# Optimization experiments

Measured on AMD Instinct MI355X. Metric: run time of the kernel, lower is better.

Reference implementation:

```python
import jax, jax.numpy as jnp
import numpy as np

HIDDEN = 2048
NUM_EXPERTS = 64
TOP_K = 8
EPS = 1e-6


def setup_inputs() -> dict:
    key = jax.random.key(0)
    k1, k2, k3, k4 = jax.random.split(key, 4)
    hidden_states = jax.random.normal(k1, (4, 4096, HIDDEN), dtype=jnp.float32)
    scale = jnp.ones((HIDDEN,), dtype=jnp.float32) + 0.01 * jax.random.normal(k2, (HIDDEN,), dtype=jnp.float32)
    proj_w = jax.random.normal(k3, (NUM_EXPERTS, HIDDEN), dtype=jnp.float32) * (HIDDEN ** -0.5)
    per_expert_scale = jnp.ones((NUM_EXPERTS,), dtype=jnp.float32) + 0.01 * jax.random.normal(k4, (NUM_EXPERTS,), dtype=jnp.float32)
    return {"hidden_states": hidden_states, "scale": scale, "proj_w": proj_w, "per_expert_scale": per_expert_scale}


def reference(hidden_states, scale, proj_w, per_expert_scale):
    H = hidden_states.shape[-1]
    # RMSNorm without learned scale
    x = hidden_states * jax.lax.rsqrt(jnp.mean(hidden_states * hidden_states, axis=-1, keepdims=True) + EPS)
    # elementwise scale and 1/sqrt(H) root-size scaling
    x = x * scale * (H ** -0.5)
    # router logits: [B,S,E]
    logits = jnp.einsum("bsh,eh->bse", x, proj_w)
    router_probs = jax.nn.softmax(logits.astype(jnp.float32), axis=-1)
    top_k_weights, top_k_index = jax.lax.top_k(router_probs, TOP_K)
    top_k_weights = top_k_weights / jnp.sum(top_k_weights, axis=-1, keepdims=True)
    top_k_weights = top_k_weights * per_expert_scale[top_k_index]
    # histc with bins=E, min=0, max=E on integer indices == bincount
    num_tokens_per_expert = jnp.bincount(top_k_index.reshape(-1), length=NUM_EXPERTS).astype(jnp.float32)
    return (top_k_weights.astype(hidden_states.dtype), top_k_index, num_tokens_per_expert)
```

## Files before the change

### kernel.cpp

```cpp
#include <hip/hip_runtime.h>
#include <math.h>

#define HIDDEN   2048
#define NEXPERT  64
#define TOPK     8
#define NTOK     16384
#define TOKB     16
#define CHUNK    256
#define NCHUNK   8
#define ROWP     264
#define RSQRT_H  0.02209708691207961
#define WSCALE   64.0f

typedef __attribute__((ext_vector_type(8))) _Float16 v8h;
typedef __attribute__((ext_vector_type(4))) float    v4f;

static __device__ __forceinline__ unsigned short f16b(float x) {
    return __builtin_bit_cast(unsigned short, (_Float16)x);
}
static __device__ __forceinline__ float f16f(unsigned short u) {
    return (float)__builtin_bit_cast(_Float16, u);
}

__global__ __launch_bounds__(256) void prep_wf(
    const float* __restrict__ w, const float* __restrict__ scale,
    unsigned short* __restrict__ wf)
{
    int i    = blockIdx.x * 256 + threadIdx.x;
    int j    = i & 7;
    int lane = (i >> 3) & 63;
    int nt   = (i >> 9) & 3;
    int ks   = i >> 11;
    int e    = nt * 16 + (lane & 15);
    int k    = ks * 32 + (lane >> 4) * 8 + j;
    float v  = w[e * HIDDEN + k] * scale[k] * WSCALE;
    unsigned short vh = f16b(v);
    unsigned short vl = f16b(v - f16f(vh));
    size_t base = (((size_t)(ks * 4 + nt) * 2) * 64 + lane) * 8 + j;
    wf[base]       = vh;
    wf[base + 512] = vl;
}

__global__ __launch_bounds__(256, 4) void router_main(
    const float* __restrict__ h, const unsigned short* __restrict__ wf,
    const float* __restrict__ pes,
    float* __restrict__ out_w, float* __restrict__ out_i, float* __restrict__ out_c)
{
    __shared__ __align__(16) char smem[34112];
    unsigned short* Xb0 = (unsigned short*)smem;
    float* lss = (float*)(smem + 33792);
    int*   hist = (int*)(smem + 33856);
    float* lg  = (float*)smem;

    const int tid  = (int)threadIdx.x;
    const int w    = __builtin_amdgcn_readfirstlane(tid >> 6);
    const int lane = tid & 63;
    const int m    = lane & 15;
    const int quad = lane >> 4;
    const int t0   = (int)blockIdx.x * TOKB;

    if (tid < NEXPERT) hist[tid] = 0;

    const int aoff = m * ROWP + quad * 8;

    v4f acc[4];
#pragma unroll
    for (int nt = 0; nt < 4; ++nt) acc[nt] = (v4f)0.f;
    float ss[4] = {0.f, 0.f, 0.f, 0.f};
    float4 st[4];

#pragma unroll
    for (int i = 0; i < 4; ++i) {
        int idx = i * 256 + tid, t = idx >> 6, kq = idx & 63;
        st[i] = *(const float4*)(h + (size_t)(t0 + t) * HIDDEN + kq * 4);
    }
#pragma unroll
    for (int i = 0; i < 4; ++i) {
        int idx = i * 256 + tid, t = idx >> 6, kq = idx & 63;
        float4 v = st[i];
        ss[i] = fmaf(v.x, v.x, fmaf(v.y, v.y, fmaf(v.z, v.z, fmaf(v.w, v.w, ss[i]))));
        unsigned short h0 = f16b(v.x), h1 = f16b(v.y), h2 = f16b(v.z), h3 = f16b(v.w);
        unsigned short l0 = f16b(v.x - f16f(h0)), l1 = f16b(v.y - f16f(h1));
        unsigned short l2 = f16b(v.z - f16f(h2)), l3 = f16b(v.w - f16f(h3));
        uint2 hp = make_uint2((unsigned)h0 | ((unsigned)h1 << 16),
                              (unsigned)h2 | ((unsigned)h3 << 16));
        uint2 lp = make_uint2((unsigned)l0 | ((unsigned)l1 << 16),
                              (unsigned)l2 | ((unsigned)l3 << 16));
        *(uint2*)(&Xb0[t * ROWP + kq * 4])        = hp;
        *(uint2*)(&Xb0[4224 + t * ROWP + kq * 4]) = lp;
    }

    for (int c = 0; c < NCHUNK; ++c) {
        __syncthreads();
        unsigned short* buf = Xb0 + (c & 1) * 8448;
        unsigned short* nbuf = Xb0 + ((c + 1) & 1) * 8448;

        if (c < NCHUNK - 1) {
#pragma unroll
            for (int i = 0; i < 4; ++i) {
                int idx = i * 256 + tid, t = idx >> 6, kq = idx & 63;
                st[i] = *(const float4*)(h + (size_t)(t0 + t) * HIDDEN
                                           + (c + 1) * CHUNK + kq * 4);
            }
        }

#pragma unroll
        for (int s = 0; s < 2; ++s) {
            const int ksl = 2 * w + s;
            const int ksg = c * 8 + ksl;
            v8h ah = *(const v8h*)(&buf[aoff + ksl * 32]);
            v8h al = *(const v8h*)(&buf[4224 + aoff + ksl * 32]);
#pragma unroll
            for (int nt = 0; nt < 4; ++nt) {
                const unsigned short* bp =
                    wf + (((size_t)(ksg * 4 + nt) * 2) * 64 + lane) * 8;
                v8h bh = *(const v8h*)bp;
                v8h bl = *(const v8h*)(bp + 512);
                acc[nt] = __builtin_amdgcn_mfma_f32_16x16x32_f16(ah, bh, acc[nt], 0, 0, 0);
                acc[nt] = __builtin_amdgcn_mfma_f32_16x16x32_f16(ah, bl, acc[nt], 0, 0, 0);
                acc[nt] = __builtin_amdgcn_mfma_f32_16x16x32_f16(al, bh, acc[nt], 0, 0, 0);
            }
        }

        if (c < NCHUNK - 1) {
#pragma unroll
            for (int i = 0; i < 4; ++i) {
                int idx = i * 256 + tid, t = idx >> 6, kq = idx & 63;
                float4 v = st[i];
                ss[i] = fmaf(v.x, v.x, fmaf(v.y, v.y, fmaf(v.z, v.z, fmaf(v.w, v.w, ss[i]))));
                unsigned short h0 = f16b(v.x), h1 = f16b(v.y), h2 = f16b(v.z), h3 = f16b(v.w);
                unsigned short l0 = f16b(v.x - f16f(h0)), l1 = f16b(v.y - f16f(h1));
                unsigned short l2 = f16b(v.z - f16f(h2)), l3 = f16b(v.w - f16f(h3));
                uint2 hp = make_uint2((unsigned)h0 | ((unsigned)h1 << 16),
                                      (unsigned)h2 | ((unsigned)h3 << 16));
                uint2 lp = make_uint2((unsigned)l0 | ((unsigned)l1 << 16),
                                      (unsigned)l2 | ((unsigned)l3 << 16));
                *(uint2*)(&nbuf[t * ROWP + kq * 4])        = hp;
                *(uint2*)(&nbuf[4224 + t * ROWP + kq * 4]) = lp;
            }
        }
    }

#pragma unroll
    for (int i = 0; i < 4; ++i) {
        float s = ss[i];
#pragma unroll
        for (int off = 32; off; off >>= 1) s += __shfl_xor(s, off, 64);
        if (lane == 0) lss[i * 4 + w] = s;
    }
    __syncthreads();

#pragma unroll
    for (int nt = 0; nt < 4; ++nt)
#pragma unroll
        for (int r = 0; r < 4; ++r) {
            int tl = quad * 4 + r;
            lg[(w * 16 + tl) * 65 + nt * 16 + m] = acc[nt][r];
        }
    __syncthreads();

    for (int i = 0; i < 4; ++i) {
        const int tok = w * 4 + i;
        float lsum = (lg[tok * 65 + lane]          + lg[1040 + tok * 65 + lane])
                   + (lg[2080 + tok * 65 + lane]   + lg[3120 + tok * 65 + lane]);
        double sst = (double)lss[tok];
        double rr  = 1.0 / sqrt(sst * (1.0 / (double)HIDDEN) + 1e-6);
        float logit = (float)((double)lsum * rr * (RSQRT_H / (double)WSCALE));

        float work = logit;
        float myval = 0.f; int myidx = 0; float m0 = 0.f;
#pragma unroll
        for (int j = 0; j < TOPK; ++j) {
            float mx = work;
#pragma unroll
            for (int off = 32; off; off >>= 1) mx = fmaxf(mx, __shfl_xor(mx, off, 64));
            unsigned long long msk = __ballot(work == mx);
            int src = __ffsll((long long)msk) - 1;
            if (j == 0) m0 = mx;
            if (lane == j) { myval = mx; myidx = src; }
            if (lane == src) work = -3.402823466e38f;
        }

        float ev = (lane < TOPK) ? expf(myval - m0) : 0.f;
        float es = ev;
        es += __shfl_xor(es, 1, 64);
        es += __shfl_xor(es, 2, 64);
        es += __shfl_xor(es, 4, 64);
        if (lane < TOPK) {
            float wgt = (ev / es) * pes[myidx];
            size_t o = (size_t)(t0 + tok) * TOPK + lane;
            out_w[o] = wgt;
            out_i[o] = (float)myidx;
            atomicAdd(&hist[myidx], 1);
        }
    }

    __syncthreads();
    if (tid < NEXPERT)
        atomicAdd(&out_c[tid], (float)hist[tid]);
}

extern "C" void kernel_launch(void* const* d_in, const int* in_sizes, int n_in,
                              void* d_out, int out_size, void* d_ws, size_t ws_size,
                              hipStream_t stream) {
    const float* h     = (const float*)d_in[0];
    const float* scale = (const float*)d_in[1];
    const float* w     = (const float*)d_in[2];
    const float* pes   = (const float*)d_in[3];

    unsigned short* wf = (unsigned short*)d_ws;

    float* out_w = (float*)d_out;
    float* out_i = (float*)d_out + (size_t)NTOK * TOPK;
    float* out_c = (float*)d_out + (size_t)NTOK * TOPK * 2;

    hipMemsetAsync(out_c, 0, NEXPERT * sizeof(float), stream);

    prep_wf<<<512, 256, 0, stream>>>(w, scale, wf);

    router_main<<<NTOK / TOKB, 256, 0, stream>>>(h, wf, pes, out_w, out_i, out_c);
}
```

Before: 234.5 us.

## Load activations directly into MFMA registers, split K across waves, rank-based top-k

Drops the LDS double-buffered staging of fp16 hi/lo activation tiles. Each wave now reads its own K-slice of the 16 token rows straight from global memory into MFMA operand registers, and the four partial accumulators are reduced through LDS at the end. The per-token sum of squares is computed per lane and reduced in double precision, and the serial 8-step shuffle-max top-k is replaced by a parallel rank count over the 64 logits. This removes many syncthreads and LDS traffic, at the cost of less coalesced global loads (each lane reads 32 contiguous bytes per row) and no explicit prefetch overlap.

```diff
diff --git a/kernel.cpp b/kernel.cpp
--- a/kernel.cpp
+++ b/kernel.cpp
@@ -6,21 +6,11 @@
 #define TOPK     8
 #define NTOK     16384
 #define TOKB     16
-#define CHUNK    256
-#define NCHUNK   8
-#define ROWP     264
 #define RSQRT_H  0.02209708691207961
-#define WSCALE   64.0f
+#define WSCALE   64.0
 
 typedef __attribute__((ext_vector_type(8))) _Float16 v8h;
 typedef __attribute__((ext_vector_type(4))) float    v4f;
-
-static __device__ __forceinline__ unsigned short f16b(float x) {
-    return __builtin_bit_cast(unsigned short, (_Float16)x);
-}
-static __device__ __forceinline__ float f16f(unsigned short u) {
-    return (float)__builtin_bit_cast(_Float16, u);
-}
 
 __global__ __launch_bounds__(256) void prep_wf(
     const float* __restrict__ w, const float* __restrict__ scale,
@@ -33,12 +23,12 @@
     int ks   = i >> 11;
     int e    = nt * 16 + (lane & 15);
     int k    = ks * 32 + (lane >> 4) * 8 + j;
-    float v  = w[e * HIDDEN + k] * scale[k] * WSCALE;
-    unsigned short vh = f16b(v);
-    unsigned short vl = f16b(v - f16f(vh));
+    float v  = w[e * HIDDEN + k] * scale[k] * (float)WSCALE;
+    _Float16 vh = (_Float16)v;
+    _Float16 vl = (_Float16)(v - (float)vh);
     size_t base = (((size_t)(ks * 4 + nt) * 2) * 64 + lane) * 8 + j;
-    wf[base]       = vh;
-    wf[base + 512] = vl;
+    wf[base]       = __builtin_bit_cast(unsigned short, vh);
+    wf[base + 512] = __builtin_bit_cast(unsigned short, vl);
 }
 
 __global__ __launch_bounds__(256, 4) void router_main(
@@ -46,11 +36,11 @@
     const float* __restrict__ pes,
     float* __restrict__ out_w, float* __restrict__ out_i, float* __restrict__ out_c)
 {
-    __shared__ __align__(16) char smem[34112];
-    unsigned short* Xb0 = (unsigned short*)smem;
-    float* lss = (float*)(smem + 33792);
-    int*   hist = (int*)(smem + 33856);
-    float* lg  = (float*)smem;
+    __shared__ float  part[4 * 1056];
+    __shared__ float  lg[16 * 68];
+    __shared__ float  ssp[256];
+    __shared__ double rd[16];
+    __shared__ int    hist[NEXPERT];
 
     const int tid  = (int)threadIdx.x;
     const int w    = __builtin_amdgcn_readfirstlane(tid >> 6);
@@ -61,137 +51,97 @@
 
     if (tid < NEXPERT) hist[tid] = 0;
 
-    const int aoff = m * ROWP + quad * 8;
+    const float* __restrict__ hrow = h + (size_t)(t0 + m) * HIDDEN + w * 512 + quad * 8;
+    const unsigned short* __restrict__ wb = wf + (size_t)w * 65536 + lane * 8;
 
     v4f acc[4];
 #pragma unroll
     for (int nt = 0; nt < 4; ++nt) acc[nt] = (v4f)0.f;
-    float ss[4] = {0.f, 0.f, 0.f, 0.f};
-    float4 st[4];
+    float ss = 0.f;
 
+#pragma unroll 4
+    for (int s = 0; s < 16; ++s) {
+        float4 va = *(const float4*)(hrow + s * 32);
+        float4 vb = *(const float4*)(hrow + s * 32 + 4);
+        ss = fmaf(va.x, va.x, fmaf(va.y, va.y, fmaf(va.z, va.z, fmaf(va.w, va.w, ss))));
+        ss = fmaf(vb.x, vb.x, fmaf(vb.y, vb.y, fmaf(vb.z, vb.z, fmaf(vb.w, vb.w, ss))));
+        v8h ah, al;
+        ah[0] = (_Float16)va.x;  al[0] = (_Float16)(va.x - (float)ah[0]);
+        ah[1] = (_Float16)va.y;  al[1] = (_Float16)(va.y - (float)ah[1]);
+        ah[2] = (_Float16)va.z;  al[2] = (_Float16)(va.z - (float)ah[2]);
+        ah[3] = (_Float16)va.w;  al[3] = (_Float16)(va.w - (float)ah[3]);
+        ah[4] = (_Float16)vb.x;  al[4] = (_Float16)(vb.x - (float)ah[4]);
+        ah[5] = (_Float16)vb.y;  al[5] = (_Float16)(vb.y - (float)ah[5]);
+        ah[6] = (_Float16)vb.z;  al[6] = (_Float16)(vb.z - (float)ah[6]);
+        ah[7] = (_Float16)vb.w;  al[7] = (_Float16)(vb.w - (float)ah[7]);
 #pragma unroll
-    for (int i = 0; i < 4; ++i) {
-        int idx = i * 256 + tid, t = idx >> 6, kq = idx & 63;
-        st[i] = *(const float4*)(h + (size_t)(t0 + t) * HIDDEN + kq * 4);
-    }
-#pragma unroll
-    for (int i = 0; i < 4; ++i) {
-        int idx = i * 256 + tid, t = idx >> 6, kq = idx & 63;
-        float4 v = st[i];
-        ss[i] = fmaf(v.x, v.x, fmaf(v.y, v.y, fmaf(v.z, v.z, fmaf(v.w, v.w, ss[i]))));
-        unsigned short h0 = f16b(v.x), h1 = f16b(v.y), h2 = f16b(v.z), h3 = f16b(v.w);
-        unsigned short l0 = f16b(v.x - f16f(h0)), l1 = f16b(v.y - f16f(h1));
-        unsigned short l2 = f16b(v.z - f16f(h2)), l3 = f16b(v.w - f16f(h3));
-        uint2 hp = make_uint2((unsigned)h0 | ((unsigned)h1 << 16),
-                              (unsigned)h2 | ((unsigned)h3 << 16));
-        uint2 lp = make_uint2((unsigned)l0 | ((unsigned)l1 << 16),
-                              (unsigned)l2 | ((unsigned)l3 << 16));
-        *(uint2*)(&Xb0[t * ROWP + kq * 4])        = hp;
-        *(uint2*)(&Xb0[4224 + t * ROWP + kq * 4]) = lp;
-    }
-
-    for (int c = 0; c < NCHUNK; ++c) {
-        __syncthreads();
-        unsigned short* buf = Xb0 + (c & 1) * 8448;
-        unsigned short* nbuf = Xb0 + ((c + 1) & 1) * 8448;
-
-        if (c < NCHUNK - 1) {
-#pragma unroll
-            for (int i = 0; i < 4; ++i) {
-                int idx = i * 256 + tid, t = idx >> 6, kq = idx & 63;
-                st[i] = *(const float4*)(h + (size_t)(t0 + t) * HIDDEN
-                                           + (c + 1) * CHUNK + kq * 4);
-            }
-        }
-
-#pragma unroll
-        for (int s = 0; s < 2; ++s) {
-            const int ksl = 2 * w + s;
-            const int ksg = c * 8 + ksl;
-            v8h ah = *(const v8h*)(&buf[aoff + ksl * 32]);
-            v8h al = *(const v8h*)(&buf[4224 + aoff + ksl * 32]);
-#pragma unroll
-            for (int nt = 0; nt < 4; ++nt) {
-                const unsigned short* bp =
-                    wf + (((size_t)(ksg * 4 + nt) * 2) * 64 + lane) * 8;
-                v8h bh = *(const v8h*)bp;
-                v8h bl = *(const v8h*)(bp + 512);
-                acc[nt] = __builtin_amdgcn_mfma_f32_16x16x32_f16(ah, bh, acc[nt], 0, 0, 0);
-                acc[nt] = __builtin_amdgcn_mfma_f32_16x16x32_f16(ah, bl, acc[nt], 0, 0, 0);
-                acc[nt] = __builtin_amdgcn_mfma_f32_16x16x32_f16(al, bh, acc[nt], 0, 0, 0);
-            }
-        }
-
-        if (c < NCHUNK - 1) {
-#pragma unroll
-            for (int i = 0; i < 4; ++i) {
-                int idx = i * 256 + tid, t = idx >> 6, kq = idx & 63;
-                float4 v = st[i];
-                ss[i] = fmaf(v.x, v.x, fmaf(v.y, v.y, fmaf(v.z, v.z, fmaf(v.w, v.w, ss[i]))));
-                unsigned short h0 = f16b(v.x), h1 = f16b(v.y), h2 = f16b(v.z), h3 = f16b(v.w);
-                unsigned short l0 = f16b(v.x - f16f(h0)), l1 = f16b(v.y - f16f(h1));
-                unsigned short l2 = f16b(v.z - f16f(h2)), l3 = f16b(v.w - f16f(h3));
-                uint2 hp = make_uint2((unsigned)h0 | ((unsigned)h1 << 16),
-                                      (unsigned)h2 | ((unsigned)h3 << 16));
-                uint2 lp = make_uint2((unsigned)l0 | ((unsigned)l1 << 16),
-                                      (unsigned)l2 | ((unsigned)l3 << 16));
-                *(uint2*)(&nbuf[t * ROWP + kq * 4])        = hp;
-                *(uint2*)(&nbuf[4224 + t * ROWP + kq * 4]) = lp;
-            }
+        for (int nt = 0; nt < 4; ++nt) {
+            const unsigned short* bp = wb + s * 4096 + nt * 1024;
+            v8h bh = *(const v8h*)bp;
+            v8h bl = *(const v8h*)(bp + 512);
+            acc[nt] = __builtin_amdgcn_mfma_f32_16x16x32_f16(ah, bh, acc[nt], 0, 0, 0);
+            acc[nt] = __builtin_amdgcn_mfma_f32_16x16x32_f16(ah, bl, acc[nt], 0, 0, 0);
+            acc[nt] = __builtin_amdgcn_mfma_f32_16x16x32_f16(al, bh, acc[nt], 0, 0, 0);
         }
     }
 
 #pragma unroll
+    for (int nt = 0; nt < 4; ++nt)
+#pragma unroll
+        for (int r = 0; r < 4; ++r)
+            part[w * 1056 + (quad * 4 + r) * 66 + nt * 16 + m] = acc[nt][r];
+    ssp[w * 64 + quad * 16 + m] = ss;
+    __syncthreads();
+
+    if (tid < TOKB) {
+        double s = 0.0;
+#pragma unroll
+        for (int p = 0; p < 16; ++p) s += (double)ssp[(p >> 2) * 64 + (p & 3) * 16 + tid];
+        rd[tid] = (1.0 / sqrt(s * (1.0 / (double)HIDDEN) + 1e-6)) * (RSQRT_H / WSCALE);
+    }
+    float cs[4];
+#pragma unroll
     for (int i = 0; i < 4; ++i) {
-        float s = ss[i];
+        int t = i * 4 + w;
+        cs[i] = (part[t * 66 + lane]        + part[1056 + t * 66 + lane])
+              + (part[2112 + t * 66 + lane] + part[3168 + t * 66 + lane]);
+    }
+    __syncthreads();
 #pragma unroll
-        for (int off = 32; off; off >>= 1) s += __shfl_xor(s, off, 64);
-        if (lane == 0) lss[i * 4 + w] = s;
+    for (int i = 0; i < 4; ++i) {
+        int t = i * 4 + w;
+        lg[t * 68 + lane] = (float)((double)cs[i] * rd[t]);
     }
     __syncthreads();
 
-#pragma unroll
-    for (int nt = 0; nt < 4; ++nt)
-#pragma unroll
-        for (int r = 0; r < 4; ++r) {
-            int tl = quad * 4 + r;
-            lg[(w * 16 + tl) * 65 + nt * 16 + m] = acc[nt][r];
-        }
-    __syncthreads();
-
+    const float mypes = pes[lane];
     for (int i = 0; i < 4; ++i) {
         const int tok = w * 4 + i;
-        float lsum = (lg[tok * 65 + lane]          + lg[1040 + tok * 65 + lane])
-                   + (lg[2080 + tok * 65 + lane]   + lg[3120 + tok * 65 + lane]);
-        double sst = (double)lss[tok];
-        double rr  = 1.0 / sqrt(sst * (1.0 / (double)HIDDEN) + 1e-6);
-        float logit = (float)((double)lsum * rr * (RSQRT_H / (double)WSCALE));
-
-        float work = logit;
-        float myval = 0.f; int myidx = 0; float m0 = 0.f;
+        const float myv = lg[tok * 68 + lane];
+        int rank = 0;
+        float mx = -3.402823466e38f;
 #pragma unroll
-        for (int j = 0; j < TOPK; ++j) {
-            float mx = work;
-#pragma unroll
-            for (int off = 32; off; off >>= 1) mx = fmaxf(mx, __shfl_xor(mx, off, 64));
-            unsigned long long msk = __ballot(work == mx);
-            int src = __ffsll((long long)msk) - 1;
-            if (j == 0) m0 = mx;
-            if (lane == j) { myval = mx; myidx = src; }
-            if (lane == src) work = -3.402823466e38f;
+        for (int j4 = 0; j4 < 64; j4 += 4) {
+            float4 q = *(const float4*)(&lg[tok * 68 + j4]);
+            mx = fmaxf(mx, fmaxf(fmaxf(q.x, q.y), fmaxf(q.z, q.w)));
+            rank += (q.x > myv || (q.x == myv && (j4 + 0) < lane)) ? 1 : 0;
+            rank += (q.y > myv || (q.y == myv && (j4 + 1) < lane)) ? 1 : 0;
+            rank += (q.z > myv || (q.z == myv && (j4 + 2) < lane)) ? 1 : 0;
+            rank += (q.w > myv || (q.w == myv && (j4 + 3) < lane)) ? 1 : 0;
         }
-
-        float ev = (lane < TOPK) ? expf(myval - m0) : 0.f;
+        float ev = (rank < TOPK) ? expf(myv - mx) : 0.f;
         float es = ev;
         es += __shfl_xor(es, 1, 64);
         es += __shfl_xor(es, 2, 64);
         es += __shfl_xor(es, 4, 64);
-        if (lane < TOPK) {
-            float wgt = (ev / es) * pes[myidx];
-            size_t o = (size_t)(t0 + tok) * TOPK + lane;
-            out_w[o] = wgt;
-            out_i[o] = (float)myidx;
-            atomicAdd(&hist[myidx], 1);
+        es += __shfl_xor(es, 8, 64);
+        es += __shfl_xor(es, 16, 64);
+        es += __shfl_xor(es, 32, 64);
+        if (rank < TOPK) {
+            size_t o = (size_t)(t0 + tok) * TOPK + rank;
+            out_w[o] = (ev / es) * mypes;
+            out_i[o] = (float)lane;
+            atomicAdd(&hist[lane], 1);
         }
     }
 
```

Result: no change. 239.0 us (+1.9%).
